# Kernel tuning notes

Measured on AMD Instinct MI355X. Metric: run time of the kernel, lower is better.

The kernel has to match this reference:

```python
import jax, jax.numpy as jnp
import numpy as np
from functools import partial

VOCAB, EMB = 32000, 512
HIDDEN = (1024, 512, 256)
OUT = 7
S, T = 1024, 64  # S = scan (seq) axis, T = 'timesteps' (effective batch)


def _lstm_layer(x, Wih, Whh, bih, bhh):
    """PyTorch-semantics LSTM over axis 0. x: (S, B, E) -> hs: (S, B, H)."""
    B = x.shape[1]
    H = Whh.shape[1]
    # precompute input contribution to all gates: (S, B, 4H)
    xg = jnp.einsum('sbe,ge->sbg', x, Wih) + bih + bhh

    def step(carry, xg_t):
        h, c = carry
        gates = xg_t + h @ Whh.T  # (B, 4H)
        i, f, g, o = jnp.split(gates, 4, axis=-1)  # torch gate order i,f,g,o
        i = jax.nn.sigmoid(i)
        f = jax.nn.sigmoid(f)
        g = jnp.tanh(g)
        o = jax.nn.sigmoid(o)
        c = f * c + i * g
        h = o * jnp.tanh(c)
        return (h, c), h

    init = (jnp.zeros((B, H), x.dtype), jnp.zeros((B, H), x.dtype))
    _, hs = jax.lax.scan(step, init, xg)
    return hs


def setup_inputs():
    key = jax.random.key(0)
    ks = jax.random.split(key, 16)
    inp = {
        'tokens': jax.random.randint(ks[0], (S, T), 0, VOCAB),
        'emb': jax.random.normal(ks[1], (VOCAB, EMB), jnp.float32) * 0.02,
    }
    dims = [(EMB, HIDDEN[0]), (HIDDEN[0], HIDDEN[1]), (HIDDEN[1], HIDDEN[2])]
    for li, (e, h) in enumerate(dims):
        s = 1.0 / np.sqrt(h)
        inp[f'Wih{li}'] = jax.random.uniform(ks[2 + 4 * li], (4 * h, e), jnp.float32, -s, s)
        inp[f'Whh{li}'] = jax.random.uniform(ks[3 + 4 * li], (4 * h, h), jnp.float32, -s, s)
        inp[f'bih{li}'] = jax.random.uniform(ks[4 + 4 * li], (4 * h,), jnp.float32, -s, s)
        inp[f'bhh{li}'] = jax.random.uniform(ks[5 + 4 * li], (4 * h,), jnp.float32, -s, s)
    s = 1.0 / np.sqrt(HIDDEN[2])
    inp['Wlin'] = jax.random.uniform(ks[14], (OUT, HIDDEN[2]), jnp.float32, -s, s)
    inp['blin'] = jax.random.uniform(ks[15], (OUT,), jnp.float32, -s, s)
    return inp


def reference(tokens, emb, Wih0, Whh0, bih0, bhh0, Wih1, Whh1, bih1, bhh1,
              Wih2, Whh2, bih2, bhh2, Wlin, blin):
    x = emb[tokens]                                  # (S, T, EMB)
    h = _lstm_layer(x, Wih0, Whh0, bih0, bhh0)       # (S, T, 1024)
    h = _lstm_layer(h, Wih1, Whh1, bih1, bhh1)       # (S, T, 512)
    h = _lstm_layer(h, Wih2, Whh2, bih2, bhh2)       # (S, T, 256)
    last = h[:, T - 1, :]                            # out[:, timesteps-1, :]
    out = last @ Wlin.T + blin                       # (S, OUT); dropout is identity in eval
    return out
```

## Files before the change

### kernel.cpp

```cpp
#include <hip/hip_runtime.h>
#include <math.h>

#define SLEN 1024

__device__ __forceinline__ float sigf(float x) { return 1.0f / (1.0f + __expf(-x)); }

__device__ __forceinline__ float agent_ld(const float* p) {
  return __hip_atomic_load(p, __ATOMIC_RELAXED, __HIP_MEMORY_SCOPE_AGENT);
}
__device__ __forceinline__ void agent_st(float* p, float v) {
  __hip_atomic_store(p, v, __ATOMIC_RELAXED, __HIP_MEMORY_SCOPE_AGENT);
}
__device__ __forceinline__ bool is_sent(float f) { return __float_as_uint(f) == 0xFFFFFFFFu; }

__global__ void embed_k(const int* __restrict__ tokens, const float* __restrict__ emb,
                        float* __restrict__ x) {
  const int t = blockIdx.x;
  const int tok = tokens[t * 64 + 63];
  const float4 v = ((const float4*)(emb + (size_t)tok * 512))[threadIdx.x];
  ((float4*)(x + (size_t)t * 512))[threadIdx.x] = v;
}

template<int HOUT, int EIN, bool POLL_IN>
__device__ void lstm_role(int ublk,
                          const float* __restrict__ Wih, const float* __restrict__ Whh,
                          const float* __restrict__ bih, const float* __restrict__ bhh,
                          const float* __restrict__ in_hist, float* __restrict__ hout) {
  constexpr int C     = EIN + HOUT;
  constexpr int SLOTS = C / 256;
  constexpr int XQ    = EIN / 4;
  constexpr int EPN   = EIN / 512;
  constexpr int HPN   = (HOUT >= 512) ? (HOUT / 512) : 1;
  constexpr bool HGUARD = (HOUT < 512);

  __shared__ __align__(16) float in_lds[C];
  __shared__ float g_raw[32];

  const int tid = threadIdx.x;
  const int c   = tid & 63;
  const int r2  = tid >> 6;
  const int u0  = ublk * 8;

  float4 wreg[4][SLOTS];
  #pragma unroll
  for (int rr = 0; rr < 4; ++rr) {
    const int lr = 4 * r2 + rr;
    const int gi = lr >> 3, ui = lr & 7;
    const size_t grow = (size_t)gi * HOUT + (size_t)(u0 + ui);
    const float4* wih4 = (const float4*)(Wih + grow * EIN);
    const float4* whh4 = (const float4*)(Whh + grow * HOUT);
    #pragma unroll
    for (int s = 0; s < SLOTS; ++s) {
      const int c4 = s * 64 + c;
      wreg[rr][s] = (c4 < XQ) ? wih4[c4] : whh4[c4 - XQ];
    }
  }

  float b0 = 0.f, b1 = 0.f, b2 = 0.f, b3 = 0.f, cst = 0.f;
  if (tid < 8) {
    b0 = bih[0*HOUT + u0 + tid] + bhh[0*HOUT + u0 + tid];
    b1 = bih[1*HOUT + u0 + tid] + bhh[1*HOUT + u0 + tid];
    b2 = bih[2*HOUT + u0 + tid] + bhh[2*HOUT + u0 + tid];
    b3 = bih[3*HOUT + u0 + tid] + bhh[3*HOUT + u0 + tid];
  }

  for (int t = 0; t < SLEN; ++t) {
    float ev[EPN];
    float hv[HPN];
    const float* esrc = in_hist + (size_t)t * EIN + EPN * tid;
    const float* hsrc = hout + (size_t)((t > 0 ? t : 1) - 1) * HOUT + HPN * tid;
    const bool hon   = (!HGUARD) || (tid * HPN < HOUT);
    const bool hneed = (t > 0) && hon;

    if constexpr (POLL_IN) {
      for (;;) {
        bool ok = true;
        #pragma unroll
        for (int i = 0; i < EPN; ++i) ev[i] = agent_ld(esrc + i);
        if (hneed) {
          #pragma unroll
          for (int i = 0; i < HPN; ++i) hv[i] = agent_ld(hsrc + i);
          #pragma unroll
          for (int i = 0; i < HPN; ++i) ok &= !is_sent(hv[i]);
        }
        #pragma unroll
        for (int i = 0; i < EPN; ++i) ok &= !is_sent(ev[i]);
        if (ok) break;
        __builtin_amdgcn_s_sleep(2);
      }
    } else {
      #pragma unroll
      for (int i = 0; i < EPN; ++i) ev[i] = esrc[i];
      if (hneed) {
        for (;;) {
          bool ok = true;
          #pragma unroll
          for (int i = 0; i < HPN; ++i) hv[i] = agent_ld(hsrc + i);
          #pragma unroll
          for (int i = 0; i < HPN; ++i) ok &= !is_sent(hv[i]);
          if (ok) break;
          __builtin_amdgcn_s_sleep(2);
        }
      }
    }

    #pragma unroll
    for (int i = 0; i < EPN; ++i) in_lds[EPN * tid + i] = ev[i];
    if (hon) {
      #pragma unroll
      for (int i = 0; i < HPN; ++i) in_lds[EIN + HPN * tid + i] = hneed ? hv[i] : 0.0f;
    }
    __syncthreads();

    float a0 = 0.f, a1 = 0.f, a2 = 0.f, a3 = 0.f;
    #pragma unroll
    for (int s = 0; s < SLOTS; ++s) {
      const float4 iv = ((const float4*)in_lds)[s * 64 + c];
      a0 += wreg[0][s].x*iv.x + wreg[0][s].y*iv.y + wreg[0][s].z*iv.z + wreg[0][s].w*iv.w;
      a1 += wreg[1][s].x*iv.x + wreg[1][s].y*iv.y + wreg[1][s].z*iv.z + wreg[1][s].w*iv.w;
      a2 += wreg[2][s].x*iv.x + wreg[2][s].y*iv.y + wreg[2][s].z*iv.z + wreg[2][s].w*iv.w;
      a3 += wreg[3][s].x*iv.x + wreg[3][s].y*iv.y + wreg[3][s].z*iv.z + wreg[3][s].w*iv.w;
    }
    #pragma unroll
    for (int off = 32; off > 0; off >>= 1) {
      a0 += __shfl_xor(a0, off);
      a1 += __shfl_xor(a1, off);
      a2 += __shfl_xor(a2, off);
      a3 += __shfl_xor(a3, off);
    }
    if (c == 0) {
      g_raw[4*r2 + 0] = a0; g_raw[4*r2 + 1] = a1;
      g_raw[4*r2 + 2] = a2; g_raw[4*r2 + 3] = a3;
    }
    __syncthreads();

    if (tid < 8) {
      const float I = sigf(g_raw[      tid] + b0);
      const float F = sigf(g_raw[ 8 +  tid] + b1);
      const float G = tanhf(g_raw[16 + tid] + b2);
      const float O = sigf(g_raw[24 + tid] + b3);
      cst = F * cst + I * G;
      agent_st(hout + (size_t)t * HOUT + u0 + tid, O * tanhf(cst));
    }
    __syncthreads();
  }
}

__device__ void final_role(int fb, const float* __restrict__ h2,
                           const float* __restrict__ Wlin, const float* __restrict__ blin,
                           float* __restrict__ out) {
  const int tid = threadIdx.x;
  float wl[7];
  #pragma unroll
  for (int o = 0; o < 7; ++o) wl[o] = 0.f;
  if (tid < 256) {
    #pragma unroll
    for (int o = 0; o < 7; ++o) wl[o] = Wlin[o * 256 + tid];
  }
  __shared__ float red[4][7];
  for (int t = fb; t < SLEN; t += 8) {
    float h = 0.0f;
    if (tid < 256) {
      h = agent_ld(h2 + (size_t)t * 256 + tid);
      while (is_sent(h)) {
        __builtin_amdgcn_s_sleep(2);
        h = agent_ld(h2 + (size_t)t * 256 + tid);
      }
    }
    float p[7];
    #pragma unroll
    for (int o = 0; o < 7; ++o) p[o] = h * wl[o];
    #pragma unroll
    for (int off = 32; off > 0; off >>= 1) {
      #pragma unroll
      for (int o = 0; o < 7; ++o) p[o] += __shfl_xor(p[o], off);
    }
    const int w = tid >> 6;
    if (w < 4 && (tid & 63) == 0) {
      #pragma unroll
      for (int o = 0; o < 7; ++o) red[w][o] = p[o];
    }
    __syncthreads();
    if (tid == 0) {
      #pragma unroll
      for (int o = 0; o < 7; ++o)
        out[t * 7 + o] = red[0][o] + red[1][o] + red[2][o] + red[3][o] + blin[o];
    }
    __syncthreads();
  }
}

__global__ __launch_bounds__(512, 2) void pipe_k(
    const float* __restrict__ x,
    const float* __restrict__ Wih0, const float* __restrict__ Whh0,
    const float* __restrict__ bih0, const float* __restrict__ bhh0,
    const float* __restrict__ Wih1, const float* __restrict__ Whh1,
    const float* __restrict__ bih1, const float* __restrict__ bhh1,
    const float* __restrict__ Wih2, const float* __restrict__ Whh2,
    const float* __restrict__ bih2, const float* __restrict__ bhh2,
    const float* __restrict__ Wlin, const float* __restrict__ blin,
    float* __restrict__ h0, float* __restrict__ h1, float* __restrict__ h2,
    float* __restrict__ out) {
  const int b = blockIdx.x;
  if (b < 128) {
    lstm_role<1024, 512, false>(b, Wih0, Whh0, bih0, bhh0, x, h0);
  } else if (b < 192) {
    lstm_role<512, 1024, true>(b - 128, Wih1, Whh1, bih1, bhh1, h0, h1);
  } else if (b < 224) {
    lstm_role<256, 512, true>(b - 192, Wih2, Whh2, bih2, bhh2, h1, h2);
  } else {
    final_role(b - 224, h2, Wlin, blin, out);
  }
}

extern "C" void kernel_launch(void* const* d_in, const int* in_sizes, int n_in,
                              void* d_out, int out_size, void* d_ws, size_t ws_size,
                              hipStream_t stream) {
  const int*   tokens = (const int*)  d_in[0];
  const float* emb  = (const float*)d_in[1];
  const float* Wih0 = (const float*)d_in[2];
  const float* Whh0 = (const float*)d_in[3];
  const float* bih0 = (const float*)d_in[4];
  const float* bhh0 = (const float*)d_in[5];
  const float* Wih1 = (const float*)d_in[6];
  const float* Whh1 = (const float*)d_in[7];
  const float* bih1 = (const float*)d_in[8];
  const float* bhh1 = (const float*)d_in[9];
  const float* Wih2 = (const float*)d_in[10];
  const float* Whh2 = (const float*)d_in[11];
  const float* bih2 = (const float*)d_in[12];
  const float* bhh2 = (const float*)d_in[13];
  const float* Wlin = (const float*)d_in[14];
  const float* blin = (const float*)d_in[15];

  float* x  = (float*)d_ws;
  float* h0 = x  + (size_t)1024 * 512;
  float* h1 = h0 + (size_t)1024 * 1024;
  float* h2 = h1 + (size_t)1024 * 512;

  hipMemsetAsync(h0, 0xFF,
                 ((size_t)1024*1024 + (size_t)1024*512 + (size_t)1024*256) * sizeof(float),
                 stream);
  embed_k<<<1024, 128, 0, stream>>>(tokens, emb, x);
  pipe_k<<<232, 512, 0, stream>>>(x, Wih0, Whh0, bih0, bhh0,
                                  Wih1, Whh1, bih1, bhh1,
                                  Wih2, Whh2, bih2, bhh2,
                                  Wlin, blin, h0, h1, h2, (float*)d_out);
}
```

Measured before the change: 2.655 ms.

## Assign one hidden unit per wave and double-buffer LDS to drop barriers

Each wave now owns one hidden unit and holds all four of its gate rows, so the gate nonlinearity and cell update happen in lane 0 of that wave. This removes the g_raw LDS exchange and two of the three __syncthreads per timestep. The input LDS buffer is double-buffered by timestep parity so the next step's writes cannot race with reads from the current step. The s_sleep calls in the spin-wait loops are also removed to cut polling latency, at the cost of more memory traffic and contention from busy polling.

```diff
diff --git a/kernel.cpp b/kernel.cpp
--- a/kernel.cpp
+++ b/kernel.cpp
@@ -33,35 +33,32 @@
   constexpr int HPN   = (HOUT >= 512) ? (HOUT / 512) : 1;
   constexpr bool HGUARD = (HOUT < 512);
 
-  __shared__ __align__(16) float in_lds[C];
-  __shared__ float g_raw[32];
+  __shared__ __align__(16) float in_lds[2][C];
 
   const int tid = threadIdx.x;
   const int c   = tid & 63;
-  const int r2  = tid >> 6;
-  const int u0  = ublk * 8;
+  const int w   = tid >> 6;
+  const int u   = ublk * 8 + w;
 
   float4 wreg[4][SLOTS];
   #pragma unroll
-  for (int rr = 0; rr < 4; ++rr) {
-    const int lr = 4 * r2 + rr;
-    const int gi = lr >> 3, ui = lr & 7;
-    const size_t grow = (size_t)gi * HOUT + (size_t)(u0 + ui);
+  for (int g = 0; g < 4; ++g) {
+    const size_t grow = (size_t)g * HOUT + (size_t)u;
     const float4* wih4 = (const float4*)(Wih + grow * EIN);
     const float4* whh4 = (const float4*)(Whh + grow * HOUT);
     #pragma unroll
     for (int s = 0; s < SLOTS; ++s) {
       const int c4 = s * 64 + c;
-      wreg[rr][s] = (c4 < XQ) ? wih4[c4] : whh4[c4 - XQ];
-    }
-  }
-
-  float b0 = 0.f, b1 = 0.f, b2 = 0.f, b3 = 0.f, cst = 0.f;
-  if (tid < 8) {
-    b0 = bih[0*HOUT + u0 + tid] + bhh[0*HOUT + u0 + tid];
-    b1 = bih[1*HOUT + u0 + tid] + bhh[1*HOUT + u0 + tid];
-    b2 = bih[2*HOUT + u0 + tid] + bhh[2*HOUT + u0 + tid];
-    b3 = bih[3*HOUT + u0 + tid] + bhh[3*HOUT + u0 + tid];
+      wreg[g][s] = (c4 < XQ) ? wih4[c4] : whh4[c4 - XQ];
+    }
+  }
+
+  float bg0 = 0.f, bg1 = 0.f, bg2 = 0.f, bg3 = 0.f, cst = 0.f;
+  if (c == 0) {
+    bg0 = bih[0*HOUT + u] + bhh[0*HOUT + u];
+    bg1 = bih[1*HOUT + u] + bhh[1*HOUT + u];
+    bg2 = bih[2*HOUT + u] + bhh[2*HOUT + u];
+    bg3 = bih[3*HOUT + u] + bhh[3*HOUT + u];
   }
 
   for (int t = 0; t < SLEN; ++t) {
@@ -86,7 +83,6 @@
         #pragma unroll
         for (int i = 0; i < EPN; ++i) ok &= !is_sent(ev[i]);
         if (ok) break;
-        __builtin_amdgcn_s_sleep(2);
       }
     } else {
       #pragma unroll
@@ -99,23 +95,24 @@
           #pragma unroll
           for (int i = 0; i < HPN; ++i) ok &= !is_sent(hv[i]);
           if (ok) break;
-          __builtin_amdgcn_s_sleep(2);
         }
       }
     }
 
-    #pragma unroll
-    for (int i = 0; i < EPN; ++i) in_lds[EPN * tid + i] = ev[i];
+    float* dst = in_lds[t & 1];
+    #pragma unroll
+    for (int i = 0; i < EPN; ++i) dst[EPN * tid + i] = ev[i];
     if (hon) {
       #pragma unroll
-      for (int i = 0; i < HPN; ++i) in_lds[EIN + HPN * tid + i] = hneed ? hv[i] : 0.0f;
+      for (int i = 0; i < HPN; ++i) dst[EIN + HPN * tid + i] = hneed ? hv[i] : 0.0f;
     }
     __syncthreads();
 
     float a0 = 0.f, a1 = 0.f, a2 = 0.f, a3 = 0.f;
+    const float4* iv4 = (const float4*)dst;
     #pragma unroll
     for (int s = 0; s < SLOTS; ++s) {
-      const float4 iv = ((const float4*)in_lds)[s * 64 + c];
+      const float4 iv = iv4[s * 64 + c];
       a0 += wreg[0][s].x*iv.x + wreg[0][s].y*iv.y + wreg[0][s].z*iv.z + wreg[0][s].w*iv.w;
       a1 += wreg[1][s].x*iv.x + wreg[1][s].y*iv.y + wreg[1][s].z*iv.z + wreg[1][s].w*iv.w;
       a2 += wreg[2][s].x*iv.x + wreg[2][s].y*iv.y + wreg[2][s].z*iv.z + wreg[2][s].w*iv.w;
@@ -129,20 +126,13 @@
       a3 += __shfl_xor(a3, off);
     }
     if (c == 0) {
-      g_raw[4*r2 + 0] = a0; g_raw[4*r2 + 1] = a1;
-      g_raw[4*r2 + 2] = a2; g_raw[4*r2 + 3] = a3;
-    }
-    __syncthreads();
-
-    if (tid < 8) {
-      const float I = sigf(g_raw[      tid] + b0);
-      const float F = sigf(g_raw[ 8 +  tid] + b1);
-      const float G = tanhf(g_raw[16 + tid] + b2);
-      const float O = sigf(g_raw[24 + tid] + b3);
+      const float I = sigf(a0 + bg0);
+      const float F = sigf(a1 + bg1);
+      const float G = tanhf(a2 + bg2);
+      const float O = sigf(a3 + bg3);
       cst = F * cst + I * G;
-      agent_st(hout + (size_t)t * HOUT + u0 + tid, O * tanhf(cst));
-    }
-    __syncthreads();
+      agent_st(hout + (size_t)t * HOUT + u, O * tanhf(cst));
+    }
   }
 }
 
@@ -163,7 +153,6 @@
     if (tid < 256) {
       h = agent_ld(h2 + (size_t)t * 256 + tid);
       while (is_sent(h)) {
-        __builtin_amdgcn_s_sleep(2);
         h = agent_ld(h2 + (size_t)t * 256 + tid);
       }
     }
```

Result: slower. 5.199 ms (+95.8%).
